# Kernel optimization log

Measured on AMD Instinct MI355X. Metric: run time of the kernel, lower is better.

The kernel has to match this reference:

```python
import jax, jax.numpy as jnp
import numpy as np

N_NODES = 100000
N_EDGES = 400000
IN_DIM = 100
OUT_DIM = 200
NUM_STEPS = 4


def setup_inputs() -> dict:
    key = jax.random.key(0)
    ks = jax.random.split(key, 8)
    x = jax.random.normal(ks[0], (N_NODES, IN_DIM), dtype=jnp.float32)
    edge_index = jax.random.randint(ks[1], (2, N_EDGES), 0, N_NODES, dtype=jnp.int64)
    s = 0.05
    W = jax.random.normal(ks[2], (NUM_STEPS, OUT_DIM, OUT_DIM), dtype=jnp.float32) * s
    w_ih = jax.random.normal(ks[3], (3 * OUT_DIM, OUT_DIM), dtype=jnp.float32) * s
    w_hh = jax.random.normal(ks[4], (3 * OUT_DIM, OUT_DIM), dtype=jnp.float32) * s
    b_ih = jax.random.normal(ks[5], (3 * OUT_DIM,), dtype=jnp.float32) * s
    b_hh = jax.random.normal(ks[6], (3 * OUT_DIM,), dtype=jnp.float32) * s
    cls_w = jax.random.normal(ks[7], (2, OUT_DIM), dtype=jnp.float32) * s
    cls_b = jnp.zeros((2,), dtype=jnp.float32)
    return {"x": x, "W": W, "w_ih": w_ih, "w_hh": w_hh, "b_ih": b_ih,
            "b_hh": b_hh, "cls_w": cls_w, "cls_b": cls_b, "edge_index": edge_index}


def _gru_cell(a, h, w_ih, w_hh, b_ih, b_hh):
    # torch.nn.GRUCell math: input a, hidden h
    gi = a @ w_ih.T + b_ih          # [N, 3D]
    gh = h @ w_hh.T + b_hh          # [N, 3D]
    i_r, i_z, i_n = jnp.split(gi, 3, axis=1)
    h_r, h_z, h_n = jnp.split(gh, 3, axis=1)
    r = jax.nn.sigmoid(i_r + h_r)
    z = jax.nn.sigmoid(i_z + h_z)
    n = jnp.tanh(i_n + r * h_n)
    return (1.0 - z) * n + z * h


def reference(x, W, w_ih, w_hh, b_ih, b_hh, cls_w, cls_b, edge_index):
    N = x.shape[0]
    # GatedGraphConv pads input features with zeros up to out_channels
    h = jnp.pad(x, ((0, 0), (0, OUT_DIM - x.shape[1])))
    src, dst = edge_index[0], edge_index[1]
    for i in range(NUM_STEPS):
        m = h @ W[i]                                         # [N, D]
        aggr = jax.ops.segment_sum(m[src], dst, num_segments=N)  # scatter-add
        h = _gru_cell(aggr, h, w_ih, w_hh, b_ih, b_hh)
    out = jax.nn.relu(h)
    # global_max_pool with all-zero batch ids -> max over all nodes
    pooled = jnp.max(out, axis=0, keepdims=True)             # [1, D]
    logits = pooled @ cls_w.T + cls_b                        # [1, 2]
    return jax.nn.softmax(logits, axis=1)
```

## Files before the change

### kernel.cpp

```cpp
#include <hip/hip_runtime.h>
#include <hip/hip_bf16.h>
#include <math.h>

#define N_NODES 100000
#define N_PAD   100096
#define N_EDGES 400000
#define IN_DIM  100
#define D       200
#define DP      208
#define KP      224
#define NUM_STEPS 4

#define TILE_SHORTS  21504
#define HALF_SHORTS  10752
#define HALF_GROUPS  21

typedef __attribute__((ext_vector_type(8))) short bfrag;
typedef __attribute__((ext_vector_type(4))) float facc;

__device__ float g_Wc[NUM_STEPS * 600 * D];
__device__ short g_Wall[NUM_STEPS * 13 * TILE_SHORTS];
__device__ float g_bias[6 * DP];

__device__ __forceinline__ float fast_sigmoid(float x) {
    return __builtin_amdgcn_rcpf(1.0f + __expf(-x));
}
__device__ __forceinline__ float fast_tanh(float x) {
    return 2.0f * __builtin_amdgcn_rcpf(1.0f + __expf(-2.0f * x)) - 1.0f;
}
__device__ __forceinline__ float bf2f(short u) {
    unsigned int x = ((unsigned int)(unsigned short)u) << 16;
    return __uint_as_float(x);
}

__global__ __launch_bounds__(256) void wc_kernel(const float* __restrict__ W,
                                                 const float* __restrict__ w_ih) {
    int s = blockIdx.x / 600;
    int j = blockIdx.x % 600;
    int k = threadIdx.x;
    if (k >= D) return;
    const float* wr = &w_ih[(size_t)j * D];
    const float* Wr = &W[(size_t)s * D * D + (size_t)k * D];
    float acc = 0.0f;
    #pragma unroll 4
    for (int t = 0; t < D; ++t) acc += wr[t] * Wr[t];
    g_Wc[((size_t)s * 600 + j) * D + k] = acc;
}

__global__ __launch_bounds__(256) void wconv_kernel(const float* __restrict__ w_hh) {
    int idx = blockIdx.x * 256 + threadIdx.x;
    int l  = idx & 63;
    int t  = (idx >> 6) % 7;
    int g  = (idx / 448) % 6;
    int jt = (idx / 2688) % 13;
    int s  = idx / 34944;
    int j  = jt * 16 + (l & 15);
    int k0 = t * 32 + (l >> 4) * 8;
    short* out = g_Wall + (size_t)idx * 8;
    #pragma unroll
    for (int i = 0; i < 8; ++i) {
        int k = k0 + i;
        float v = 0.0f;
        if (j < D && k < D)
            v = (g < 3) ? g_Wc[((size_t)s * 600 + g * 200 + j) * D + k]
                        : w_hh[((size_t)(g - 3) * 200 + j) * D + k];
        __hip_bfloat16 b = __float2bfloat16(v);
        out[i] = *reinterpret_cast<short*>(&b);
    }
}

__global__ void bias_kernel(const float* __restrict__ b_ih, const float* __restrict__ b_hh) {
    int idx = blockIdx.x * 256 + threadIdx.x;
    if (idx >= 6 * DP) return;
    int g = idx / DP, j = idx % DP;
    float v = 0.0f;
    if (j < D) v = (g < 3) ? b_ih[g * 200 + j] : b_hh[(g - 3) * 200 + j];
    g_bias[idx] = v;
}

__global__ void pad_kernel(const float* __restrict__ x, __hip_bfloat16* __restrict__ h) {
    int idx = blockIdx.x * 256 + threadIdx.x;
    int n = idx / KP, c = idx % KP;
    float v = (n < N_NODES && c < IN_DIM) ? x[n * IN_DIM + c] : 0.0f;
    h[idx] = __float2bfloat16(v);
}

__global__ void count_kernel(const int* __restrict__ dst, int* __restrict__ cnt) {
    int e = blockIdx.x * blockDim.x + threadIdx.x;
    if (e < N_EDGES) atomicAdd(&cnt[dst[e]], 1);
}

#define SCAN_B 1024
__global__ __launch_bounds__(SCAN_B) void scan1(const int* __restrict__ cnt,
                                                int* __restrict__ incl, int* __restrict__ bsum) {
    __shared__ int ws[16];
    int i = blockIdx.x * SCAN_B + threadIdx.x;
    int lane = threadIdx.x & 63, wid = threadIdx.x >> 6;
    int v = (i < N_NODES) ? cnt[i] : 0;
    int s = v;
    #pragma unroll
    for (int o = 1; o < 64; o <<= 1) {
        int t = __shfl_up(s, o, 64);
        if (lane >= o) s += t;
    }
    if (lane == 63) ws[wid] = s;
    __syncthreads();
    if (wid == 0) {
        int t = (lane < 16) ? ws[lane] : 0;
        #pragma unroll
        for (int o = 1; o < 16; o <<= 1) {
            int u = __shfl_up(t, o, 64);
            if (lane >= o) t += u;
        }
        if (lane < 16) ws[lane] = t;
    }
    __syncthreads();
    if (wid > 0) s += ws[wid - 1];
    if (i < N_NODES) incl[i] = s;
    if (threadIdx.x == SCAN_B - 1) bsum[blockIdx.x] = s;
}
__global__ void scan2(int* __restrict__ bsum, int nb) {
    __shared__ int sh[128];
    int v = (threadIdx.x < nb) ? bsum[threadIdx.x] : 0;
    sh[threadIdx.x] = v; __syncthreads();
    for (int off = 1; off < 128; off <<= 1) {
        int t = (threadIdx.x >= off) ? sh[threadIdx.x - off] : 0;
        __syncthreads();
        sh[threadIdx.x] += t;
        __syncthreads();
    }
    if (threadIdx.x < nb) bsum[threadIdx.x] = sh[threadIdx.x] - v;
}
__global__ void scan3(const int* __restrict__ cnt, const int* __restrict__ incl,
                      const int* __restrict__ bsum, int* __restrict__ off,
                      int* __restrict__ cursor) {
    int i = blockIdx.x * blockDim.x + threadIdx.x;
    if (i < N_NODES) {
        int v = incl[i] - cnt[i] + bsum[i / SCAN_B];
        off[i] = v; cursor[i] = v;
    }
    if (i == 0) off[N_NODES] = N_EDGES;
}
__global__ void fill_kernel(const int* __restrict__ src, const int* __restrict__ dst,
                            int* __restrict__ cursor, int* __restrict__ esrc) {
    int e = blockIdx.x * blockDim.x + threadIdx.x;
    if (e < N_EDGES) {
        int pos = atomicAdd(&cursor[dst[e]], 1);
        esrc[pos] = src[e];
    }
}

__device__ __forceinline__ void stage_half(const short* __restrict__ gsrc,
                                           short* lds_dst, int wave, int lane) {
    #pragma unroll
    for (int g = wave; g < HALF_GROUPS; g += 4) {
        __builtin_amdgcn_global_load_lds(
            (const __attribute__((address_space(1))) void*)(gsrc + g * 512 + lane * 8),
            (__attribute__((address_space(3))) void*)(lds_dst + g * 512),
            16, 0, 0);
    }
}

__global__ __launch_bounds__(256, 2) void gru_fused(const __hip_bfloat16* __restrict__ hcur,
                                                    __hip_bfloat16* __restrict__ hnext,
                                                    const int* __restrict__ off,
                                                    const int* __restrict__ esrc,
                                                    unsigned int* __restrict__ pooled,
                                                    int step) {
    __shared__ short Bs[2][HALF_SHORTS];
    __shared__ unsigned int pmax[DP];
    int tid = threadIdx.x;
    int lane = tid & 63, wave = tid >> 6;
    int wbase = blockIdx.x * 128 + wave * 32;
    int mrow = lane & 15, kq = lane >> 4;
    bool dopool = (step == NUM_STEPS - 1);

    if (dopool) for (int c = tid; c < DP; c += 256) pmax[c] = 0u;

    short* LDSbase = &Bs[0][0];
    short* Awave = LDSbase + wave * 16 * KP;

    bfrag av[2][7], hv[2][7];

    int r4 = lane >> 4;
    int ck = lane & 15;
    int colA = ck * 8;
    int colB = colA + 128;
    bool sumB = (ck < 9);
    #pragma unroll
    for (int p = 0; p < 2; ++p) {
        #pragma unroll
        for (int it = 0; it < 4; ++it) {
            int rr = it * 4 + r4;
            int n = wbase + p * 16 + rr;
            float a[8] = {0, 0, 0, 0, 0, 0, 0, 0};
            float b[8] = {0, 0, 0, 0, 0, 0, 0, 0};
            if (n < N_NODES) {
                int e0 = off[n], e1 = off[n + 1];
                int e = e0;
                for (; e + 1 < e1; e += 2) {
                    size_t s0 = (size_t)esrc[e] * KP;
                    size_t s1 = (size_t)esrc[e + 1] * KP;
                    bfrag va0 = *(const bfrag*)(hcur + s0 + colA);
                    bfrag va1 = *(const bfrag*)(hcur + s1 + colA);
                    if (sumB) {
                        bfrag vb0 = *(const bfrag*)(hcur + s0 + colB);
                        bfrag vb1 = *(const bfrag*)(hcur + s1 + colB);
                        #pragma unroll
                        for (int q = 0; q < 8; ++q)
                            b[q] += bf2f(vb0[q]) + bf2f(vb1[q]);
                    }
                    #pragma unroll
                    for (int q = 0; q < 8; ++q)
                        a[q] += bf2f(va0[q]) + bf2f(va1[q]);
                }
                if (e < e1) {
                    size_t s0 = (size_t)esrc[e] * KP;
                    bfrag va0 = *(const bfrag*)(hcur + s0 + colA);
                    if (sumB) {
                        bfrag vb0 = *(const bfrag*)(hcur + s0 + colB);
                        #pragma unroll
                        for (int q = 0; q < 8; ++q) b[q] += bf2f(vb0[q]);
                    }
                    #pragma unroll
                    for (int q = 0; q < 8; ++q) a[q] += bf2f(va0[q]);
                }
            }
            __hip_bfloat16 oa[8], ob[8];
            #pragma unroll
            for (int q = 0; q < 8; ++q) {
                oa[q] = __float2bfloat16(a[q]);
                ob[q] = __float2bfloat16(b[q]);
            }
            *(ushort4*)(Awave + rr * KP + colA)     = *(const ushort4*)&oa[0];
            *(ushort4*)(Awave + rr * KP + colA + 4) = *(const ushort4*)&oa[4];
            if (ck < 12) {
                *(ushort4*)(Awave + rr * KP + colB)     = *(const ushort4*)&ob[0];
                *(ushort4*)(Awave + rr * KP + colB + 4) = *(const ushort4*)&ob[4];
            }
        }
        #pragma unroll
        for (int t = 0; t < 7; ++t)
            av[p][t] = *(const bfrag*)&Awave[mrow * KP + t * 32 + kq * 8];
    }

    size_t hbase = (size_t)(wbase + mrow) * KP + kq * 8;
    #pragma unroll
    for (int mf = 0; mf < 2; ++mf)
        #pragma unroll
        for (int t = 0; t < 7; ++t)
            hv[mf][t] = *(const bfrag*)(hcur + hbase + mf * 16 * KP + t * 32);

    const short* Wstep = g_Wall + (size_t)step * 13 * TILE_SHORTS;
    int jcol = lane & 15;
    int rowq = (lane >> 4) * 4;

    __syncthreads();
    stage_half(Wstep, &Bs[0][0], wave, lane);

    facc acc[6][2];
    unsigned short hold_u[2][4];

    for (int hk = 0; hk < 26; ++hk) {
        __syncthreads();
        if (hk + 1 < 26)
            stage_half(Wstep + (size_t)(hk + 1) * HALF_SHORTS,
                       &Bs[(hk + 1) & 1][0], wave, lane);

        int jt = hk >> 1;
        int j = jt * 16 + jcol;
        const short* Bcur = &Bs[hk & 1][0];

        if ((hk & 1) == 0) {
            #pragma unroll
            for (int mf = 0; mf < 2; ++mf)
                #pragma unroll
                for (int r = 0; r < 4; ++r)
                    hold_u[mf][r] = *(const unsigned short*)
                        (hcur + (size_t)(wbase + mf * 16 + rowq + r) * KP + j);
            #pragma unroll
            for (int g = 0; g < 6; ++g)
                #pragma unroll
                for (int mf = 0; mf < 2; ++mf) acc[g][mf] = (facc)(0.0f);
            #pragma unroll
            for (int t = 0; t < 7; ++t) {
                bfrag bv[3];
                #pragma unroll
                for (int g = 0; g < 3; ++g)
                    bv[g] = *(const bfrag*)&Bcur[(size_t)(((g * 7 + t) * 64) + lane) * 8];
                #pragma unroll
                for (int g = 0; g < 3; ++g)
                    #pragma unroll
                    for (int mf = 0; mf < 2; ++mf)
                        acc[g][mf] = __builtin_amdgcn_mfma_f32_16x16x32_bf16(av[mf][t], bv[g], acc[g][mf], 0, 0, 0);
            }
        } else {
            #pragma unroll
            for (int t = 0; t < 7; ++t) {
                bfrag bv[3];
                #pragma unroll
                for (int g = 0; g < 3; ++g)
                    bv[g] = *(const bfrag*)&Bcur[(size_t)(((g * 7 + t) * 64) + lane) * 8];
                #pragma unroll
                for (int g = 0; g < 3; ++g)
                    #pragma unroll
                    for (int mf = 0; mf < 2; ++mf)
                        acc[g + 3][mf] = __builtin_amdgcn_mfma_f32_16x16x32_bf16(hv[mf][t], bv[g], acc[g + 3][mf], 0, 0, 0);
            }

            float tmax = 0.0f;
            if (j < D) {
                float bir = g_bias[j],          biz = g_bias[DP + j],     bin = g_bias[2 * DP + j];
                float bhr = g_bias[3 * DP + j], bhz = g_bias[4 * DP + j], bhn = g_bias[5 * DP + j];
                #pragma unroll
                for (int mf = 0; mf < 2; ++mf) {
                    int m0 = wbase + mf * 16 + rowq;
                    #pragma unroll
                    for (int r = 0; r < 4; ++r) {
                        int m = m0 + r;
                        if (m < N_NODES) {
                            float hold = bf2f((short)hold_u[mf][r]);
                            float rr = fast_sigmoid(acc[0][mf][r] + bir + acc[3][mf][r] + bhr);
                            float zz = fast_sigmoid(acc[1][mf][r] + biz + acc[4][mf][r] + bhz);
                            float nn = fast_tanh(acc[2][mf][r] + bin + rr * (acc[5][mf][r] + bhn));
                            float hv2 = (1.0f - zz) * nn + zz * hold;
                            hnext[(size_t)m * KP + j] = __float2bfloat16(hv2);
                            if (hv2 > tmax) tmax = hv2;
                        }
                    }
                }
                if (dopool) atomicMax(&pmax[j], __float_as_uint(tmax));
            }
        }
    }

    if (dopool) {
        __syncthreads();
        for (int c = tid; c < D; c += 256) atomicMax(&pooled[c], pmax[c]);
    }
}

__global__ void head_kernel(const unsigned int* __restrict__ pooled,
                            const float* __restrict__ cls_w,
                            const float* __restrict__ cls_b,
                            float* __restrict__ out) {
    if (threadIdx.x == 0) {
        float l0 = cls_b[0], l1 = cls_b[1];
        for (int d = 0; d < D; ++d) {
            float p = __uint_as_float(pooled[d]);
            l0 += p * cls_w[d];
            l1 += p * cls_w[D + d];
        }
        float mx = l0 > l1 ? l0 : l1;
        float e0 = expf(l0 - mx), e1 = expf(l1 - mx);
        out[0] = e0 / (e0 + e1);
        out[1] = e1 / (e0 + e1);
    }
}

extern "C" void kernel_launch(void* const* d_in, const int* in_sizes, int n_in,
                              void* d_out, int out_size, void* d_ws, size_t ws_size,
                              hipStream_t stream) {
    const float* x     = (const float*)d_in[0];
    const float* W     = (const float*)d_in[1];
    const float* w_ih  = (const float*)d_in[2];
    const float* w_hh  = (const float*)d_in[3];
    const float* b_ih  = (const float*)d_in[4];
    const float* b_hh  = (const float*)d_in[5];
    const float* cls_w = (const float*)d_in[6];
    const float* cls_b = (const float*)d_in[7];
    const int*   ei    = (const int*)d_in[8];
    const int* src = ei;
    const int* dst = ei + N_EDGES;

    const size_t ROWB = (size_t)N_PAD * KP;
    __hip_bfloat16* hA   = (__hip_bfloat16*)d_ws;
    __hip_bfloat16* hB   = hA + ROWB;
    int* cnt    = (int*)(hB + ROWB);
    int* incl   = cnt + N_NODES;
    int* bsum   = incl + N_NODES;
    int* off    = bsum + 128;
    int* cursor = off + N_NODES + 1;
    int* esrc   = cursor + N_NODES;
    unsigned int* pooled = (unsigned int*)(esrc + N_EDGES);

    hipMemsetAsync(cnt, 0, N_NODES * sizeof(int), stream);
    count_kernel<<<(N_EDGES + 255) / 256, 256, 0, stream>>>(dst, cnt);
    scan1<<<(N_NODES + SCAN_B - 1) / SCAN_B, SCAN_B, 0, stream>>>(cnt, incl, bsum);
    scan2<<<1, 128, 0, stream>>>(bsum, (N_NODES + SCAN_B - 1) / SCAN_B);
    scan3<<<(N_NODES + 255) / 256, 256, 0, stream>>>(cnt, incl, bsum, off, cursor);
    fill_kernel<<<(N_EDGES + 255) / 256, 256, 0, stream>>>(src, dst, cursor, esrc);

    wc_kernel<<<NUM_STEPS * 600, 256, 0, stream>>>(W, w_ih);
    wconv_kernel<<<(NUM_STEPS * 13 * 6 * 7 * 64) / 256, 256, 0, stream>>>(w_hh);
    bias_kernel<<<(6 * DP + 255) / 256, 256, 0, stream>>>(b_ih, b_hh);

    pad_kernel<<<(int)(ROWB / 256), 256, 0, stream>>>(x, hA);
    hipMemsetAsync(pooled, 0, D * sizeof(unsigned int), stream);

    __hip_bfloat16* hcur = hA;
    __hip_bfloat16* hnext = hB;
    for (int s = 0; s < NUM_STEPS; ++s) {
        gru_fused<<<N_PAD / 128, 256, 0, stream>>>(hcur, hnext, off, esrc, pooled, s);
        __hip_bfloat16* t = hcur; hcur = hnext; hnext = t;
    }
    head_kernel<<<1, 64, 0, stream>>>(pooled, cls_w, cls_b, (float*)d_out);
}
```

Baseline: 892.7 us.

## Load-balance neighbor gather with atomic row queue and LDS-cached edge indices

Replaces the fixed per-wave row assignment in the neighbor-aggregation phase with a block-wide atomic work counter: 32-lane groups take rows dynamically, and each lane handles 8 contiguous feature columns across the full row width. A block's edge source indices are staged in LDS when they fit, and the edge loop is unrolled by four to raise memory-level parallelism. Aggregated rows go to a shared scratch area, and the waves that own each half load their A fragments from it after a barrier. This targets load imbalance from uneven node degrees and the repeated global index loads. In exchange it adds extra barriers, LDS traffic, atomics and some idle lanes.

```diff
diff --git a/kernel.cpp b/kernel.cpp
--- a/kernel.cpp
+++ b/kernel.cpp
@@ -14,6 +14,7 @@
 #define TILE_SHORTS  21504
 #define HALF_SHORTS  10752
 #define HALF_GROUPS  21
+#define EIDX_CAP     1536
 
 typedef __attribute__((ext_vector_type(8))) short bfrag;
 typedef __attribute__((ext_vector_type(4))) float facc;
@@ -168,80 +169,91 @@
                                                     unsigned int* __restrict__ pooled,
                                                     int step) {
     __shared__ short Bs[2][HALF_SHORTS];
+    __shared__ int eidx[EIDX_CAP];
+    __shared__ int offs[129];
+    __shared__ int rowctr;
     __shared__ unsigned int pmax[DP];
     int tid = threadIdx.x;
     int lane = tid & 63, wave = tid >> 6;
-    int wbase = blockIdx.x * 128 + wave * 32;
+    int blk0 = blockIdx.x * 128;
+    int wbase = blk0 + wave * 32;
     int mrow = lane & 15, kq = lane >> 4;
     bool dopool = (step == NUM_STEPS - 1);
 
     if (dopool) for (int c = tid; c < DP; c += 256) pmax[c] = 0u;
 
-    short* LDSbase = &Bs[0][0];
-    short* Awave = LDSbase + wave * 16 * KP;
-
+    for (int i = tid; i < 129; i += 256) {
+        int n = blk0 + i;
+        offs[i] = off[n < N_NODES ? n : N_NODES];
+    }
+    __syncthreads();
+    int lo = offs[0];
+    int cntb = offs[128] - lo;
+    bool use_lds = (cntb <= EIDX_CAP);
+    if (use_lds)
+        for (int i = tid; i < cntb; i += 256) eidx[i] = esrc[lo + i];
+
+    short* scr = &Bs[0][0] + 7168;
     bfrag av[2][7], hv[2][7];
 
-    int r4 = lane >> 4;
-    int ck = lane & 15;
+    int group_src = lane & 32;
+    int ck = tid & 31;
     int colA = ck * 8;
-    int colB = colA + 128;
-    bool sumB = (ck < 9);
+
     #pragma unroll
     for (int p = 0; p < 2; ++p) {
-        #pragma unroll
-        for (int it = 0; it < 4; ++it) {
-            int rr = it * 4 + r4;
-            int n = wbase + p * 16 + rr;
+        if (tid == 0) rowctr = 0;
+        __syncthreads();
+        for (;;) {
+            int r = 0;
+            if ((tid & 31) == 0) r = atomicAdd(&rowctr, 1);
+            r = __shfl(r, group_src, 64);
+            if (r >= 64) break;
+            int row = p * 64 + r;
+            int e0 = offs[row] - lo, e1 = offs[row + 1] - lo;
             float a[8] = {0, 0, 0, 0, 0, 0, 0, 0};
-            float b[8] = {0, 0, 0, 0, 0, 0, 0, 0};
-            if (n < N_NODES) {
-                int e0 = off[n], e1 = off[n + 1];
+            if (ck < 25) {
                 int e = e0;
-                for (; e + 1 < e1; e += 2) {
-                    size_t s0 = (size_t)esrc[e] * KP;
-                    size_t s1 = (size_t)esrc[e + 1] * KP;
-                    bfrag va0 = *(const bfrag*)(hcur + s0 + colA);
-                    bfrag va1 = *(const bfrag*)(hcur + s1 + colA);
-                    if (sumB) {
-                        bfrag vb0 = *(const bfrag*)(hcur + s0 + colB);
-                        bfrag vb1 = *(const bfrag*)(hcur + s1 + colB);
-                        #pragma unroll
-                        for (int q = 0; q < 8; ++q)
-                            b[q] += bf2f(vb0[q]) + bf2f(vb1[q]);
+                for (; e + 3 < e1; e += 4) {
+                    int i0, i1, i2, i3;
+                    if (use_lds) {
+                        i0 = eidx[e]; i1 = eidx[e + 1]; i2 = eidx[e + 2]; i3 = eidx[e + 3];
+                    } else {
+                        i0 = esrc[lo + e];     i1 = esrc[lo + e + 1];
+                        i2 = esrc[lo + e + 2]; i3 = esrc[lo + e + 3];
                     }
+                    bfrag a0 = *(const bfrag*)(hcur + (size_t)i0 * KP + colA);
+                    bfrag a1 = *(const bfrag*)(hcur + (size_t)i1 * KP + colA);
+                    bfrag a2 = *(const bfrag*)(hcur + (size_t)i2 * KP + colA);
+                    bfrag a3 = *(const bfrag*)(hcur + (size_t)i3 * KP + colA);
                     #pragma unroll
                     for (int q = 0; q < 8; ++q)
-                        a[q] += bf2f(va0[q]) + bf2f(va1[q]);
+                        a[q] += (bf2f(a0[q]) + bf2f(a1[q])) + (bf2f(a2[q]) + bf2f(a3[q]));
                 }
-                if (e < e1) {
-                    size_t s0 = (size_t)esrc[e] * KP;
-                    bfrag va0 = *(const bfrag*)(hcur + s0 + colA);
-                    if (sumB) {
-                        bfrag vb0 = *(const bfrag*)(hcur + s0 + colB);
-                        #pragma unroll
-                        for (int q = 0; q < 8; ++q) b[q] += bf2f(vb0[q]);
-                    }
+                for (; e < e1; ++e) {
+                    int i0 = use_lds ? eidx[e] : esrc[lo + e];
+                    bfrag a0 = *(const bfrag*)(hcur + (size_t)i0 * KP + colA);
                     #pragma unroll
-                    for (int q = 0; q < 8; ++q) a[q] += bf2f(va0[q]);
+                    for (int q = 0; q < 8; ++q) a[q] += bf2f(a0[q]);
                 }
             }
-            __hip_bfloat16 oa[8], ob[8];
-            #pragma unroll
-            for (int q = 0; q < 8; ++q) {
-                oa[q] = __float2bfloat16(a[q]);
-                ob[q] = __float2bfloat16(b[q]);
-            }
-            *(ushort4*)(Awave + rr * KP + colA)     = *(const ushort4*)&oa[0];
-            *(ushort4*)(Awave + rr * KP + colA + 4) = *(const ushort4*)&oa[4];
-            if (ck < 12) {
-                *(ushort4*)(Awave + rr * KP + colB)     = *(const ushort4*)&ob[0];
-                *(ushort4*)(Awave + rr * KP + colB + 4) = *(const ushort4*)&ob[4];
+            if (ck < 28) {
+                __hip_bfloat16 o[8];
+                #pragma unroll
+                for (int q = 0; q < 8; ++q) o[q] = __float2bfloat16(a[q]);
+                *(ushort4*)(scr + r * KP + colA)     = *(const ushort4*)&o[0];
+                *(ushort4*)(scr + r * KP + colA + 4) = *(const ushort4*)&o[4];
             }
         }
-        #pragma unroll
-        for (int t = 0; t < 7; ++t)
-            av[p][t] = *(const bfrag*)&Awave[mrow * KP + t * 32 + kq * 8];
+        __syncthreads();
+        if ((wave >> 1) == p) {
+            int sbase = (wave & 1) * 32;
+            #pragma unroll
+            for (int mf = 0; mf < 2; ++mf)
+                #pragma unroll
+                for (int t = 0; t < 7; ++t)
+                    av[mf][t] = *(const bfrag*)&scr[(sbase + mf * 16 + mrow) * KP + t * 32 + kq * 8];
+        }
     }
 
     size_t hbase = (size_t)(wbase + mrow) * KP + kq * 8;
```

Measured after the change: 896.2 us. Within noise of the previous version (+0.4%).
